# Optimization experiments

Hardware: AMD Instinct MI355X
Metric: run time of the kernel (lower is better)

## Reference

```python
import jax, jax.numpy as jnp
import numpy as np

B, N, DIM, H, DH = 2, 2048, 1024, 16, 64
INNER = H * DH
ROPE_BASE = 10000.0


def setup_inputs() -> dict:
    key = jax.random.key(0)
    ks = jax.random.split(key, 6)
    s = 0.02
    return {
        "x": jax.random.normal(ks[0], (B, N, DIM), jnp.float32),
        "Wq": jax.random.normal(ks[1], (DIM, INNER), jnp.float32) * s,
        "Wk": jax.random.normal(ks[2], (DIM, INNER), jnp.float32) * s,
        "Wv": jax.random.normal(ks[3], (DIM, INNER), jnp.float32) * s,
        "Wo": jax.random.normal(ks[4], (INNER, DIM), jnp.float32) * s,
        "bo": jnp.zeros((DIM,), jnp.float32),
    }


def _rotate_half(x):
    # einops '... (d r) -> ... d r' with r=2: x1 = even lanes, x2 = odd lanes,
    # then cat((-x2, x1), dim=-1)
    x1 = x[..., 0::2]
    x2 = x[..., 1::2]
    return jnp.concatenate([-x2, x1], axis=-1)


def _rope_sin_cos(n, d, dtype):
    # inv_freq over arange(0, d, 2); emb = cat(f, f) -> length d
    inv_freq = 1.0 / (ROPE_BASE ** (jnp.arange(0, d, 2, dtype=jnp.float32) / d))
    f = jnp.arange(n, dtype=jnp.float32)[:, None] * inv_freq[None, :]  # [n, d/2]
    e = jnp.concatenate([f, f], axis=-1)  # [n, d]
    return jnp.sin(e).astype(dtype), jnp.cos(e).astype(dtype)


def _apply_rope(t, sin, cos):
    # t: [b, h, n, d]; sin/cos: [n, d]; rot_dim == d (full head), t_pass empty
    return t * cos[None, None] + _rotate_half(t) * sin[None, None]


def reference(x, Wq, Wk, Wv, Wo, bo):
    b, n, _ = x.shape
    scale = DH ** (-0.5)

    def split_heads(y):  # [b, n, h*d] -> [b, h, n, d]
        return y.reshape(b, n, H, DH).transpose(0, 2, 1, 3)

    q = split_heads(x @ Wq)
    k = split_heads(x @ Wk)
    v = split_heads(x @ Wv)

    sin, cos = _rope_sin_cos(n, DH, x.dtype)
    q = _apply_rope(q, sin, cos)
    k = _apply_rope(k, sin, cos)

    # causal SDPA (mask=None path -> is_causal=True), eval mode so dropout_p=0
    scores = jnp.einsum("bhqd,bhkd->bhqk", q, k) * scale
    causal = jnp.tril(jnp.ones((n, n), dtype=bool))
    scores = jnp.where(causal[None, None], scores, jnp.finfo(scores.dtype).min)
    probs = jax.nn.softmax(scores, axis=-1)
    attn = jnp.einsum("bhqk,bhkd->bhqd", probs, v)

    out = attn.transpose(0, 2, 1, 3).reshape(b, n, INNER) @ Wo + bo
    return out, k, v
```

## Files before the change

### kernel.cpp

```cpp
#include <hip/hip_runtime.h>
#include <cstdint>
#include <cmath>

#define BB   2
#define NN   2048
#define DIMM 1024
#define NHH  16
#define DHH  64
#define MMR  (BB * NN)

typedef _Float16 half8  __attribute__((ext_vector_type(8)));
typedef _Float16 half4v __attribute__((ext_vector_type(4)));
typedef float    f32x4  __attribute__((ext_vector_type(4)));

#define GLD16(gp, lp)                                                          \
  __builtin_amdgcn_global_load_lds(                                            \
      (const __attribute__((address_space(1))) unsigned int*)(gp),             \
      (__attribute__((address_space(3))) unsigned int*)(lp), 16, 0, 0)

__global__ __launch_bounds__(256) void cvt_x_kernel(const float* __restrict__ x,
                                                    _Float16* __restrict__ xh) {
  int i = (blockIdx.x * 256 + threadIdx.x) * 4;
  float4 v = *(const float4*)(x + i);
  half4v h;
  h[0] = (_Float16)v.x; h[1] = (_Float16)v.y;
  h[2] = (_Float16)v.z; h[3] = (_Float16)v.w;
  *(half4v*)(xh + i) = h;
}

__global__ __launch_bounds__(256) void transpose_w_kernel(
    const float* __restrict__ Wq, const float* __restrict__ Wk,
    const float* __restrict__ Wv, const float* __restrict__ Wo,
    _Float16* __restrict__ wt) {
  __shared__ float tile[64][65];
  int z = blockIdx.z;
  const float* W = (z == 0) ? Wq : (z == 1) ? Wk : (z == 2) ? Wv : Wo;
  _Float16* dst = wt + (size_t)z * 1024 * 1024;
  int r0 = blockIdx.x * 64;
  int c0 = blockIdx.y * 64;
  int t = threadIdx.x;
  int tr = t >> 4;
  int tc = (t & 15) * 4;
#pragma unroll
  for (int i = 0; i < 4; ++i) {
    float4 v = *(const float4*)(W + (size_t)(r0 + tr + i * 16) * 1024 + c0 + tc);
    tile[tr + i * 16][tc + 0] = v.x;
    tile[tr + i * 16][tc + 1] = v.y;
    tile[tr + i * 16][tc + 2] = v.z;
    tile[tr + i * 16][tc + 3] = v.w;
  }
  __syncthreads();
#pragma unroll
  for (int i = 0; i < 4; ++i) {
    int nl = tr + i * 16;
    half4v hv;
    hv[0] = (_Float16)tile[tc + 0][nl];
    hv[1] = (_Float16)tile[tc + 1][nl];
    hv[2] = (_Float16)tile[tc + 2][nl];
    hv[3] = (_Float16)tile[tc + 3][nl];
    *(half4v*)(dst + (size_t)(c0 + nl) * 1024 + r0 + tc) = hv;
  }
}

__global__ __launch_bounds__(256) void gemm_qkv_kernel(
    const _Float16* __restrict__ xh, const _Float16* __restrict__ wt,
    float* __restrict__ ko, float* __restrict__ vo,
    _Float16* __restrict__ qh, _Float16* __restrict__ kh,
    _Float16* __restrict__ vth) {
  __shared__ __align__(16) _Float16 Ast[64 * 32];
  __shared__ __align__(16) _Float16 Bst[64 * 32];
  __shared__ float Cs[64][65];
  const int m0  = blockIdx.x * 64;
  const int ngl = blockIdx.y * 64;
  const int mat = ngl >> 10;
  const int n0  = ngl & 1023;
  const _Float16* wb = wt + (size_t)mat * 1024 * 1024;
  const int t = threadIdx.x;
  const int wv = t >> 6, lane = t & 63, l16 = lane & 15, quad = lane >> 4;
  const int r = t >> 2, cl = t & 3;
  const int c = cl ^ ((r >> 2) & 3);
  const _Float16* pa = xh + (size_t)(m0 + r) * 1024 + c * 8;
  const _Float16* pb = wb + (size_t)(n0 + r) * 1024 + c * 8;
  f32x4 acc[4] = {};
  const int arow = wv * 16 + l16;
  const int aoff = arow * 32 + (quad ^ ((arow >> 2) & 3)) * 8;
  for (int k0 = 0; k0 < 1024; k0 += 32) {
    __syncthreads();
    GLD16(pa + k0, Ast + wv * 512);
    GLD16(pb + k0, Bst + wv * 512);
    __syncthreads();
    half8 af = *(const half8*)(Ast + aoff);
#pragma unroll
    for (int nt = 0; nt < 4; ++nt) {
      int brow = nt * 16 + l16;
      half8 bf = *(const half8*)(Bst + brow * 32 + (quad ^ ((brow >> 2) & 3)) * 8);
      acc[nt] = __builtin_amdgcn_mfma_f32_16x16x32_f16(af, bf, acc[nt], 0, 0, 0);
    }
  }
#pragma unroll
  for (int nt = 0; nt < 4; ++nt)
#pragma unroll
    for (int rr = 0; rr < 4; ++rr)
      Cs[wv * 16 + quad * 4 + rr][nt * 16 + l16] = acc[nt][rr];
  __syncthreads();
  int lr = t >> 2;
  int cseg = (t & 3) * 16;
  int m = m0 + lr;
  int b = m >> 11;
  int pos = m & 2047;
  int h = n0 >> 6;
  int bhh = b * NHH + h;
  float vals[16];
  if (mat == 2) {
#pragma unroll
    for (int j = 0; j < 16; ++j) vals[j] = Cs[lr][cseg + j];
  } else {
    float fpos = (float)pos;
#pragma unroll
    for (int j = 0; j < 16; ++j) {
      int i = cseg + j;
      int jd = (i < 32) ? i : (i - 32);
      float invf = exp2f((float)jd * -0.41524101186092029f);
      float ang = fpos * invf;
      float sv, cv;
      sincosf(ang, &sv, &cv);
      float partner = (i < 32) ? -Cs[lr][2 * i + 1] : Cs[lr][2 * (i - 32)];
      vals[j] = Cs[lr][i] * cv + partner * sv;
    }
  }
  size_t rowb = ((size_t)bhh * NN + pos) * DHH + cseg;
  if (mat == 0) {
    half8 h0, h1;
#pragma unroll
    for (int j = 0; j < 8; ++j) { h0[j] = (_Float16)(vals[j] * 0.125f); h1[j] = (_Float16)(vals[8 + j] * 0.125f); }
    *(half8*)(qh + rowb) = h0;
    *(half8*)(qh + rowb + 8) = h1;
  } else if (mat == 1) {
#pragma unroll
    for (int j4 = 0; j4 < 4; ++j4) {
      float4 o;
      o.x = vals[j4 * 4 + 0]; o.y = vals[j4 * 4 + 1];
      o.z = vals[j4 * 4 + 2]; o.w = vals[j4 * 4 + 3];
      *(float4*)(ko + rowb + j4 * 4) = o;
    }
    half8 h0, h1;
#pragma unroll
    for (int j = 0; j < 8; ++j) { h0[j] = (_Float16)vals[j]; h1[j] = (_Float16)vals[8 + j]; }
    *(half8*)(kh + rowb) = h0;
    *(half8*)(kh + rowb + 8) = h1;
  } else {
#pragma unroll
    for (int j4 = 0; j4 < 4; ++j4) {
      float4 o;
      o.x = vals[j4 * 4 + 0]; o.y = vals[j4 * 4 + 1];
      o.z = vals[j4 * 4 + 2]; o.w = vals[j4 * 4 + 3];
      *(float4*)(vo + rowb + j4 * 4) = o;
    }
#pragma unroll
    for (int j = 0; j < 16; ++j)
      vth[((size_t)bhh * DHH + cseg + j) * NN + pos] = (_Float16)vals[j];
  }
}

__global__ __launch_bounds__(256, 2) void fattn_kernel(
    const _Float16* __restrict__ qh, const _Float16* __restrict__ kh,
    const _Float16* __restrict__ vth, _Float16* __restrict__ ah) {
  __shared__ __align__(16) _Float16 Kt[2][4096];
  __shared__ __align__(16) _Float16 Vt[2][4096];
  __shared__ __align__(16) _Float16 Pb[4][16][72];
  const int qb = 15 - (int)blockIdx.x;
  const int bh = blockIdx.y;
  const int t = threadIdx.x;
  const int wv = t >> 6, lane = t & 63, l16 = lane & 15, quad = lane >> 4;
  const int q0 = qb * 128;
  const _Float16* kg = kh + (size_t)bh * NN * DHH;
  const _Float16* vg = vth + (size_t)bh * DHH * NN;
  half8 qf[2][2];
#pragma unroll
  for (int qt2 = 0; qt2 < 2; ++qt2) {
    const _Float16* qp =
        qh + ((size_t)bh * NN + q0 + wv * 32 + qt2 * 16 + l16) * DHH + quad * 8;
    qf[qt2][0] = *(const half8*)qp;
    qf[qt2][1] = *(const half8*)(qp + 32);
  }
  half8 ones;
#pragma unroll
  for (int j = 0; j < 8; ++j) ones[j] = (_Float16)1.f;
  f32x4 o[2][4] = {};
  f32x4 ls[2] = {};
  const int ktmax = 2 * qb + 1;
#pragma unroll
  for (int iss = 0; iss < 2; ++iss) {
    int cid = iss * 256 + wv * 64 + lane;
    int row = cid >> 3;
    int c = (cid & 7) ^ (row & 7);
    GLD16(kg + (size_t)row * DHH + c * 8, &Kt[0][(iss * 256 + wv * 64) * 8]);
    GLD16(vg + (size_t)row * NN + c * 8, &Vt[0][(iss * 256 + wv * 64) * 8]);
  }
  int cur = 0;
  for (int kt = 0; kt <= ktmax; ++kt) {
    __syncthreads();
    if (kt < ktmax) {
      const _Float16* kn = kg + (size_t)(kt + 1) * 64 * DHH;
      const _Float16* vn = vg + (kt + 1) * 64;
      int nb = cur ^ 1;
#pragma unroll
      for (int iss = 0; iss < 2; ++iss) {
        int cid = iss * 256 + wv * 64 + lane;
        int row = cid >> 3;
        int c = (cid & 7) ^ (row & 7);
        GLD16(kn + (size_t)row * DHH + c * 8, &Kt[nb][(iss * 256 + wv * 64) * 8]);
        GLD16(vn + (size_t)row * NN + c * 8, &Vt[nb][(iss * 256 + wv * 64) * 8]);
      }
    }
    if (kt * 64 <= q0 + wv * 32 + 31) {
      half8 kf[4][2], vf[4][2];
      const _Float16* Kb = Kt[cur];
      const _Float16* Vb = Vt[cur];
#pragma unroll
      for (int nt = 0; nt < 4; ++nt) {
        int row = nt * 16 + l16;
        int r7 = row & 7;
        kf[nt][0] = *(const half8*)(Kb + row * 64 + ((quad ^ r7) * 8));
        kf[nt][1] = *(const half8*)(Kb + row * 64 + (((quad + 4) ^ r7) * 8));
        vf[nt][0] = *(const half8*)(Vb + row * 64 + ((quad ^ r7) * 8));
        vf[nt][1] = *(const half8*)(Vb + row * 64 + (((quad + 4) ^ r7) * 8));
      }
#pragma unroll
      for (int qt2 = 0; qt2 < 2; ++qt2) {
        int base = q0 + wv * 32 + qt2 * 16;
        if (kt * 64 <= base + 15) {
          f32x4 s4[4];
#pragma unroll
          for (int nt = 0; nt < 4; ++nt) {
            f32x4 z = {};
            z = __builtin_amdgcn_mfma_f32_16x16x32_f16(qf[qt2][0], kf[nt][0], z, 0, 0, 0);
            s4[nt] = __builtin_amdgcn_mfma_f32_16x16x32_f16(qf[qt2][1], kf[nt][1], z, 0, 0, 0);
          }
          if (kt * 64 + 63 > base) {
#pragma unroll
            for (int nt = 0; nt < 4; ++nt) {
              int key = kt * 64 + nt * 16 + l16;
#pragma unroll
              for (int r = 0; r < 4; ++r) {
                float p = (key > base + quad * 4 + r) ? 0.f : __expf(s4[nt][r]);
                Pb[wv][quad * 4 + r][nt * 16 + l16] = (_Float16)p;
              }
            }
          } else {
#pragma unroll
            for (int nt = 0; nt < 4; ++nt)
#pragma unroll
              for (int r = 0; r < 4; ++r)
                Pb[wv][quad * 4 + r][nt * 16 + l16] = (_Float16)__expf(s4[nt][r]);
          }
          asm volatile("s_waitcnt lgkmcnt(0)" ::: "memory");
          half8 pf0 = *(const half8*)&Pb[wv][l16][quad * 8];
          half8 pf1 = *(const half8*)&Pb[wv][l16][32 + quad * 8];
#pragma unroll
          for (int nt = 0; nt < 4; ++nt) {
            o[qt2][nt] = __builtin_amdgcn_mfma_f32_16x16x32_f16(pf0, vf[nt][0], o[qt2][nt], 0, 0, 0);
            o[qt2][nt] = __builtin_amdgcn_mfma_f32_16x16x32_f16(pf1, vf[nt][1], o[qt2][nt], 0, 0, 0);
          }
          ls[qt2] = __builtin_amdgcn_mfma_f32_16x16x32_f16(pf0, ones, ls[qt2], 0, 0, 0);
          ls[qt2] = __builtin_amdgcn_mfma_f32_16x16x32_f16(pf1, ones, ls[qt2], 0, 0, 0);
        }
      }
    }
    cur ^= 1;
  }
  const int b = bh >> 4, h = bh & 15;
#pragma unroll
  for (int qt2 = 0; qt2 < 2; ++qt2)
#pragma unroll
    for (int r = 0; r < 4; ++r) {
      float inv = 1.f / ls[qt2][r];
      int pos = q0 + wv * 32 + qt2 * 16 + quad * 4 + r;
      size_t ob = ((size_t)(b * NN + pos)) * DIMM + h * DHH;
#pragma unroll
      for (int nt = 0; nt < 4; ++nt)
        ah[ob + nt * 16 + l16] = (_Float16)(o[qt2][nt][r] * inv);
    }
}

__global__ __launch_bounds__(256) void gemm_out_kernel(
    const _Float16* __restrict__ ah, const _Float16* __restrict__ wot,
    const float* __restrict__ bo, float* __restrict__ out) {
  __shared__ __align__(16) _Float16 Ast[64 * 32];
  __shared__ __align__(16) _Float16 Bst[64 * 32];
  const int m0 = blockIdx.x * 64;
  const int n0 = blockIdx.y * 64;
  const int t = threadIdx.x;
  const int wv = t >> 6, lane = t & 63, l16 = lane & 15, quad = lane >> 4;
  const int r = t >> 2, cl = t & 3;
  const int c = cl ^ ((r >> 2) & 3);
  const _Float16* pa = ah + (size_t)(m0 + r) * 1024 + c * 8;
  const _Float16* pb = wot + (size_t)(n0 + r) * 1024 + c * 8;
  f32x4 acc[4] = {};
  const int arow = wv * 16 + l16;
  const int aoff = arow * 32 + (quad ^ ((arow >> 2) & 3)) * 8;
  for (int k0 = 0; k0 < 1024; k0 += 32) {
    __syncthreads();
    GLD16(pa + k0, Ast + wv * 512);
    GLD16(pb + k0, Bst + wv * 512);
    __syncthreads();
    half8 af = *(const half8*)(Ast + aoff);
#pragma unroll
    for (int nt = 0; nt < 4; ++nt) {
      int brow = nt * 16 + l16;
      half8 bf = *(const half8*)(Bst + brow * 32 + (quad ^ ((brow >> 2) & 3)) * 8);
      acc[nt] = __builtin_amdgcn_mfma_f32_16x16x32_f16(af, bf, acc[nt], 0, 0, 0);
    }
  }
#pragma unroll
  for (int nt = 0; nt < 4; ++nt) {
    int col = n0 + nt * 16 + l16;
    float bias = bo[col];
#pragma unroll
    for (int rr = 0; rr < 4; ++rr) {
      out[(size_t)(m0 + wv * 16 + quad * 4 + rr) * 1024 + col] = acc[nt][rr] + bias;
    }
  }
}

extern "C" void kernel_launch(void* const* d_in, const int* in_sizes, int n_in,
                              void* d_out, int out_size, void* d_ws, size_t ws_size,
                              hipStream_t stream) {
  (void)in_sizes; (void)n_in; (void)out_size; (void)ws_size;
  const float* x  = (const float*)d_in[0];
  const float* Wq = (const float*)d_in[1];
  const float* Wk = (const float*)d_in[2];
  const float* Wv = (const float*)d_in[3];
  const float* Wo = (const float*)d_in[4];
  const float* bo = (const float*)d_in[5];

  float* out = (float*)d_out;
  float* ko  = out + (size_t)MMR * DIMM;
  float* vo  = ko + (size_t)BB * NHH * NN * DHH;

  char* w = (char*)d_ws;
  _Float16* xh  = (_Float16*)w;
  _Float16* ah  = (_Float16*)w;
  _Float16* wt  = (_Float16*)(w + (8u << 20));
  _Float16* qh  = (_Float16*)(w + (16u << 20));
  _Float16* kh  = (_Float16*)(w + (24u << 20));
  _Float16* vth = (_Float16*)(w + (32u << 20));

  hipLaunchKernelGGL(cvt_x_kernel, dim3(4096), dim3(256), 0, stream, x, xh);
  hipLaunchKernelGGL(transpose_w_kernel, dim3(16, 16, 4), dim3(256), 0, stream,
                     Wq, Wk, Wv, Wo, wt);
  hipLaunchKernelGGL(gemm_qkv_kernel, dim3(64, 48), dim3(256), 0, stream,
                     xh, wt, ko, vo, qh, kh, vth);
  hipLaunchKernelGGL(fattn_kernel, dim3(16, 32), dim3(256), 0, stream,
                     qh, kh, vth, ah);
  hipLaunchKernelGGL(gemm_out_kernel, dim3(64, 16), dim3(256), 0, stream,
                     ah, wt + (size_t)3 * 1024 * 1024, bo, out);
}
```

Measured before the change: 235.1 us.

## Enlarge QKV and output GEMM tiles to 128x128 with 2x2 wave layout

Both GEMM kernels move from 64x64 block tiles, where each wave computes 16x64, to 128x128 block tiles, where each wave computes a 64x64 sub-tile with a 4x4 grid of MFMA accumulators. This raises arithmetic intensity per LDS load and per global fetch. The QKV epilogue now shares LDS with the staging buffers and runs two head-chunk passes so RoPE and the layout scatter still fit. The cost is more registers per thread, fewer blocks (768 and 256), lower occupancy and weaker wave-level parallelism on a large-CU GPU. The K loop is still single-buffered.

```diff
diff --git a/kernel.cpp b/kernel.cpp
--- a/kernel.cpp
+++ b/kernel.cpp
@@ -67,98 +67,124 @@
     float* __restrict__ ko, float* __restrict__ vo,
     _Float16* __restrict__ qh, _Float16* __restrict__ kh,
     _Float16* __restrict__ vth) {
-  __shared__ __align__(16) _Float16 Ast[64 * 32];
-  __shared__ __align__(16) _Float16 Bst[64 * 32];
-  __shared__ float Cs[64][65];
-  const int m0  = blockIdx.x * 64;
-  const int ngl = blockIdx.y * 64;
-  const int mat = ngl >> 10;
-  const int n0  = ngl & 1023;
+  __shared__ __align__(16) char smem[128 * 65 * 4];
+  _Float16* Ast = (_Float16*)smem;
+  _Float16* Bst = (_Float16*)(smem + 8192);
+  float (*Cs)[65] = (float(*)[65])smem;
+
+  const int m0  = blockIdx.x * 128;
+  const int mat = blockIdx.y >> 3;
+  const int n0  = (blockIdx.y & 7) * 128;
   const _Float16* wb = wt + (size_t)mat * 1024 * 1024;
   const int t = threadIdx.x;
   const int wv = t >> 6, lane = t & 63, l16 = lane & 15, quad = lane >> 4;
+  const int wr = wv >> 1, wc = wv & 1;
   const int r = t >> 2, cl = t & 3;
   const int c = cl ^ ((r >> 2) & 3);
   const _Float16* pa = xh + (size_t)(m0 + r) * 1024 + c * 8;
   const _Float16* pb = wb + (size_t)(n0 + r) * 1024 + c * 8;
-  f32x4 acc[4] = {};
-  const int arow = wv * 16 + l16;
-  const int aoff = arow * 32 + (quad ^ ((arow >> 2) & 3)) * 8;
+  f32x4 acc[4][4] = {};
+  int aoffs[4], boffs[4];
+#pragma unroll
+  for (int mi = 0; mi < 4; ++mi) {
+    int arow = wr * 64 + mi * 16 + l16;
+    aoffs[mi] = arow * 32 + (quad ^ ((arow >> 2) & 3)) * 8;
+  }
+#pragma unroll
+  for (int n = 0; n < 4; ++n) {
+    int brow = wc * 64 + n * 16 + l16;
+    boffs[n] = brow * 32 + (quad ^ ((brow >> 2) & 3)) * 8;
+  }
   for (int k0 = 0; k0 < 1024; k0 += 32) {
     __syncthreads();
     GLD16(pa + k0, Ast + wv * 512);
+    GLD16(pa + 64 * 1024 + k0, Ast + 2048 + wv * 512);
     GLD16(pb + k0, Bst + wv * 512);
-    __syncthreads();
-    half8 af = *(const half8*)(Ast + aoff);
-#pragma unroll
-    for (int nt = 0; nt < 4; ++nt) {
-      int brow = nt * 16 + l16;
-      half8 bf = *(const half8*)(Bst + brow * 32 + (quad ^ ((brow >> 2) & 3)) * 8);
-      acc[nt] = __builtin_amdgcn_mfma_f32_16x16x32_f16(af, bf, acc[nt], 0, 0, 0);
-    }
-  }
-#pragma unroll
-  for (int nt = 0; nt < 4; ++nt)
-#pragma unroll
-    for (int rr = 0; rr < 4; ++rr)
-      Cs[wv * 16 + quad * 4 + rr][nt * 16 + l16] = acc[nt][rr];
-  __syncthreads();
-  int lr = t >> 2;
-  int cseg = (t & 3) * 16;
-  int m = m0 + lr;
-  int b = m >> 11;
-  int pos = m & 2047;
-  int h = n0 >> 6;
-  int bhh = b * NHH + h;
-  float vals[16];
-  if (mat == 2) {
-#pragma unroll
-    for (int j = 0; j < 16; ++j) vals[j] = Cs[lr][cseg + j];
-  } else {
-    float fpos = (float)pos;
-#pragma unroll
-    for (int j = 0; j < 16; ++j) {
-      int i = cseg + j;
-      int jd = (i < 32) ? i : (i - 32);
-      float invf = exp2f((float)jd * -0.41524101186092029f);
-      float ang = fpos * invf;
-      float sv, cv;
-      sincosf(ang, &sv, &cv);
-      float partner = (i < 32) ? -Cs[lr][2 * i + 1] : Cs[lr][2 * (i - 32)];
-      vals[j] = Cs[lr][i] * cv + partner * sv;
-    }
-  }
-  size_t rowb = ((size_t)bhh * NN + pos) * DHH + cseg;
-  if (mat == 0) {
-    half8 h0, h1;
-#pragma unroll
-    for (int j = 0; j < 8; ++j) { h0[j] = (_Float16)(vals[j] * 0.125f); h1[j] = (_Float16)(vals[8 + j] * 0.125f); }
-    *(half8*)(qh + rowb) = h0;
-    *(half8*)(qh + rowb + 8) = h1;
-  } else if (mat == 1) {
-#pragma unroll
-    for (int j4 = 0; j4 < 4; ++j4) {
-      float4 o;
-      o.x = vals[j4 * 4 + 0]; o.y = vals[j4 * 4 + 1];
-      o.z = vals[j4 * 4 + 2]; o.w = vals[j4 * 4 + 3];
-      *(float4*)(ko + rowb + j4 * 4) = o;
-    }
-    half8 h0, h1;
-#pragma unroll
-    for (int j = 0; j < 8; ++j) { h0[j] = (_Float16)vals[j]; h1[j] = (_Float16)vals[8 + j]; }
-    *(half8*)(kh + rowb) = h0;
-    *(half8*)(kh + rowb + 8) = h1;
-  } else {
-#pragma unroll
-    for (int j4 = 0; j4 < 4; ++j4) {
-      float4 o;
-      o.x = vals[j4 * 4 + 0]; o.y = vals[j4 * 4 + 1];
-      o.z = vals[j4 * 4 + 2]; o.w = vals[j4 * 4 + 3];
-      *(float4*)(vo + rowb + j4 * 4) = o;
-    }
-#pragma unroll
-    for (int j = 0; j < 16; ++j)
-      vth[((size_t)bhh * DHH + cseg + j) * NN + pos] = (_Float16)vals[j];
+    GLD16(pb + 64 * 1024 + k0, Bst + 2048 + wv * 512);
+    __syncthreads();
+    half8 af[4], bf[4];
+#pragma unroll
+    for (int mi = 0; mi < 4; ++mi) af[mi] = *(const half8*)(Ast + aoffs[mi]);
+#pragma unroll
+    for (int n = 0; n < 4; ++n) bf[n] = *(const half8*)(Bst + boffs[n]);
+#pragma unroll
+    for (int mi = 0; mi < 4; ++mi)
+#pragma unroll
+      for (int n = 0; n < 4; ++n)
+        acc[mi][n] = __builtin_amdgcn_mfma_f32_16x16x32_f16(af[mi], bf[n], acc[mi][n], 0, 0, 0);
+  }
+  const int lr = t >> 1;
+  const int cseg = (t & 1) * 32;
+  const int m = m0 + lr;
+  const int b = m >> 11;
+  const int pos = m & 2047;
+  const float fpos = (float)pos;
+  for (int ch = 0; ch < 2; ++ch) {
+    __syncthreads();
+    if (wc == ch) {
+#pragma unroll
+      for (int mi = 0; mi < 4; ++mi)
+#pragma unroll
+        for (int n = 0; n < 4; ++n)
+#pragma unroll
+          for (int rr = 0; rr < 4; ++rr)
+            Cs[wr * 64 + mi * 16 + quad * 4 + rr][n * 16 + l16] = acc[mi][n][rr];
+    }
+    __syncthreads();
+    const int h = (n0 >> 6) + ch;
+    const int bhh = b * NHH + h;
+    float vals[32];
+    if (mat == 2) {
+#pragma unroll
+      for (int j = 0; j < 32; ++j) vals[j] = Cs[lr][cseg + j];
+    } else {
+      const bool lo = (cseg == 0);
+#pragma unroll
+      for (int j = 0; j < 32; ++j) {
+        float invf = exp2f((float)j * -0.41524101186092029f);
+        float ang = fpos * invf;
+        float sv, cv;
+        sincosf(ang, &sv, &cv);
+        float partner = lo ? -Cs[lr][2 * j + 1] : Cs[lr][2 * j];
+        vals[j] = Cs[lr][cseg + j] * cv + partner * sv;
+      }
+    }
+    size_t rowb = ((size_t)bhh * NN + pos) * DHH + cseg;
+    if (mat == 0) {
+#pragma unroll
+      for (int j8 = 0; j8 < 4; ++j8) {
+        half8 hv;
+#pragma unroll
+        for (int j = 0; j < 8; ++j) hv[j] = (_Float16)(vals[j8 * 8 + j] * 0.125f);
+        *(half8*)(qh + rowb + j8 * 8) = hv;
+      }
+    } else if (mat == 1) {
+#pragma unroll
+      for (int j4 = 0; j4 < 8; ++j4) {
+        float4 o;
+        o.x = vals[j4 * 4 + 0]; o.y = vals[j4 * 4 + 1];
+        o.z = vals[j4 * 4 + 2]; o.w = vals[j4 * 4 + 3];
+        *(float4*)(ko + rowb + j4 * 4) = o;
+      }
+#pragma unroll
+      for (int j8 = 0; j8 < 4; ++j8) {
+        half8 hv;
+#pragma unroll
+        for (int j = 0; j < 8; ++j) hv[j] = (_Float16)vals[j8 * 8 + j];
+        *(half8*)(kh + rowb + j8 * 8) = hv;
+      }
+    } else {
+#pragma unroll
+      for (int j4 = 0; j4 < 8; ++j4) {
+        float4 o;
+        o.x = vals[j4 * 4 + 0]; o.y = vals[j4 * 4 + 1];
+        o.z = vals[j4 * 4 + 2]; o.w = vals[j4 * 4 + 3];
+        *(float4*)(vo + rowb + j4 * 4) = o;
+      }
+#pragma unroll
+      for (int j = 0; j < 32; ++j)
+        vth[((size_t)bhh * DHH + cseg + j) * NN + pos] = (_Float16)vals[j];
+    }
   }
 }
 
@@ -286,41 +312,58 @@
 __global__ __launch_bounds__(256) void gemm_out_kernel(
     const _Float16* __restrict__ ah, const _Float16* __restrict__ wot,
     const float* __restrict__ bo, float* __restrict__ out) {
-  __shared__ __align__(16) _Float16 Ast[64 * 32];
-  __shared__ __align__(16) _Float16 Bst[64 * 32];
-  const int m0 = blockIdx.x * 64;
-  const int n0 = blockIdx.y * 64;
+  __shared__ __align__(16) _Float16 Ast[128 * 32];
+  __shared__ __align__(16) _Float16 Bst[128 * 32];
+  const int m0 = blockIdx.x * 128;
+  const int n0 = blockIdx.y * 128;
   const int t = threadIdx.x;
   const int wv = t >> 6, lane = t & 63, l16 = lane & 15, quad = lane >> 4;
+  const int wr = wv >> 1, wc = wv & 1;
   const int r = t >> 2, cl = t & 3;
   const int c = cl ^ ((r >> 2) & 3);
   const _Float16* pa = ah + (size_t)(m0 + r) * 1024 + c * 8;
   const _Float16* pb = wot + (size_t)(n0 + r) * 1024 + c * 8;
-  f32x4 acc[4] = {};
-  const int arow = wv * 16 + l16;
-  const int aoff = arow * 32 + (quad ^ ((arow >> 2) & 3)) * 8;
+  f32x4 acc[4][4] = {};
+  int aoffs[4], boffs[4];
+#pragma unroll
+  for (int mi = 0; mi < 4; ++mi) {
+    int arow = wr * 64 + mi * 16 + l16;
+    aoffs[mi] = arow * 32 + (quad ^ ((arow >> 2) & 3)) * 8;
+  }
+#pragma unroll
+  for (int n = 0; n < 4; ++n) {
+    int brow = wc * 64 + n * 16 + l16;
+    boffs[n] = brow * 32 + (quad ^ ((brow >> 2) & 3)) * 8;
+  }
   for (int k0 = 0; k0 < 1024; k0 += 32) {
     __syncthreads();
     GLD16(pa + k0, Ast + wv * 512);
+    GLD16(pa + 64 * 1024 + k0, Ast + 2048 + wv * 512);
     GLD16(pb + k0, Bst + wv * 512);
-    __syncthreads();
-    half8 af = *(const half8*)(Ast + aoff);
-#pragma unroll
-    for (int nt = 0; nt < 4; ++nt) {
-      int brow = nt * 16 + l16;
-      half8 bf = *(const half8*)(Bst + brow * 32 + (quad ^ ((brow >> 2) & 3)) * 8);
-      acc[nt] = __builtin_amdgcn_mfma_f32_16x16x32_f16(af, bf, acc[nt], 0, 0, 0);
-    }
-  }
-#pragma unroll
-  for (int nt = 0; nt < 4; ++nt) {
-    int col = n0 + nt * 16 + l16;
-    float bias = bo[col];
-#pragma unroll
-    for (int rr = 0; rr < 4; ++rr) {
-      out[(size_t)(m0 + wv * 16 + quad * 4 + rr) * 1024 + col] = acc[nt][rr] + bias;
-    }
-  }
+    GLD16(pb + 64 * 1024 + k0, Bst + 2048 + wv * 512);
+    __syncthreads();
+    half8 af[4], bf[4];
+#pragma unroll
+    for (int mi = 0; mi < 4; ++mi) af[mi] = *(const half8*)(Ast + aoffs[mi]);
+#pragma unroll
+    for (int n = 0; n < 4; ++n) bf[n] = *(const half8*)(Bst + boffs[n]);
+#pragma unroll
+    for (int mi = 0; mi < 4; ++mi)
+#pragma unroll
+      for (int n = 0; n < 4; ++n)
+        acc[mi][n] = __builtin_amdgcn_mfma_f32_16x16x32_f16(af[mi], bf[n], acc[mi][n], 0, 0, 0);
+  }
+#pragma unroll
+  for (int mi = 0; mi < 4; ++mi)
+#pragma unroll
+    for (int n = 0; n < 4; ++n) {
+      int col = n0 + wc * 64 + n * 16 + l16;
+      float bias = bo[col];
+#pragma unroll
+      for (int rr = 0; rr < 4; ++rr)
+        out[(size_t)(m0 + wr * 64 + mi * 16 + quad * 4 + rr) * 1024 + col] =
+            acc[mi][n][rr] + bias;
+    }
 }
 
 extern "C" void kernel_launch(void* const* d_in, const int* in_sizes, int n_in,
@@ -349,10 +392,10 @@
   hipLaunchKernelGGL(cvt_x_kernel, dim3(4096), dim3(256), 0, stream, x, xh);
   hipLaunchKernelGGL(transpose_w_kernel, dim3(16, 16, 4), dim3(256), 0, stream,
                      Wq, Wk, Wv, Wo, wt);
-  hipLaunchKernelGGL(gemm_qkv_kernel, dim3(64, 48), dim3(256), 0, stream,
+  hipLaunchKernelGGL(gemm_qkv_kernel, dim3(32, 24), dim3(256), 0, stream,
                      xh, wt, ko, vo, qh, kh, vth);
   hipLaunchKernelGGL(fattn_kernel, dim3(16, 32), dim3(256), 0, stream,
                      qh, kh, vth, ah);
-  hipLaunchKernelGGL(gemm_out_kernel, dim3(64, 16), dim3(256), 0, stream,
+  hipLaunchKernelGGL(gemm_out_kernel, dim3(32, 8), dim3(256), 0, stream,
                      ah, wt + (size_t)3 * 1024 * 1024, bo, out);
 }
```

Measured after the change: 274.4 us. 1.17x slower.

## Double-buffer GEMM K-tiles with async LDS loads and wider K step

Applied to the files above, without the earlier changes.

Both the QKV projection and output GEMM kernels now use a two-stage LDS ping-pong buffer. The next 64-wide K slice is fetched via global_load_lds while MFMAs consume the current one, with explicit vmcnt waits and raw barriers replacing the two __syncthreads per 32-wide step. The K step doubles, which halves loop iterations and barriers, and the LDS swizzle changes to an 8-way XOR. This costs 32KB of LDS per block, which may reduce occupancy, and relies on hand-placed waitcnt correctness.

```diff
diff --git a/kernel.cpp b/kernel.cpp
--- a/kernel.cpp
+++ b/kernel.cpp
@@ -67,9 +67,11 @@
     float* __restrict__ ko, float* __restrict__ vo,
     _Float16* __restrict__ qh, _Float16* __restrict__ kh,
     _Float16* __restrict__ vth) {
-  __shared__ __align__(16) _Float16 Ast[64 * 32];
-  __shared__ __align__(16) _Float16 Bst[64 * 32];
-  __shared__ float Cs[64][65];
+  __shared__ __align__(16) char smem[32768];
+  _Float16* As = (_Float16*)smem;
+  _Float16* Bs = (_Float16*)(smem + 16384);
+  float (*Cs)[65] = (float(*)[65])smem;
+
   const int m0  = blockIdx.x * 64;
   const int ngl = blockIdx.y * 64;
   const int mat = ngl >> 10;
@@ -77,25 +79,51 @@
   const _Float16* wb = wt + (size_t)mat * 1024 * 1024;
   const int t = threadIdx.x;
   const int wv = t >> 6, lane = t & 63, l16 = lane & 15, quad = lane >> 4;
-  const int r = t >> 2, cl = t & 3;
-  const int c = cl ^ ((r >> 2) & 3);
-  const _Float16* pa = xh + (size_t)(m0 + r) * 1024 + c * 8;
-  const _Float16* pb = wb + (size_t)(n0 + r) * 1024 + c * 8;
+  const int r  = t >> 3;
+  const int cl = t & 7;
+  const int csw = (cl ^ (r & 7)) * 8;
+  const _Float16* pa0 = xh + (size_t)(m0 + r) * 1024 + csw;
+  const _Float16* pa1 = pa0 + 32 * 1024;
+  const _Float16* pb0 = wb + (size_t)(n0 + r) * 1024 + csw;
+  const _Float16* pb1 = pb0 + 32 * 1024;
   f32x4 acc[4] = {};
   const int arow = wv * 16 + l16;
-  const int aoff = arow * 32 + (quad ^ ((arow >> 2) & 3)) * 8;
-  for (int k0 = 0; k0 < 1024; k0 += 32) {
-    __syncthreads();
-    GLD16(pa + k0, Ast + wv * 512);
-    GLD16(pb + k0, Bst + wv * 512);
-    __syncthreads();
-    half8 af = *(const half8*)(Ast + aoff);
+  const int a7 = arow & 7;
+  GLD16(pa0, As + wv * 512);
+  GLD16(pa1, As + 2048 + wv * 512);
+  GLD16(pb0, Bs + wv * 512);
+  GLD16(pb1, Bs + 2048 + wv * 512);
+  int cur = 0;
+  for (int k0 = 0; k0 < 1024; k0 += 64) {
+    if (k0 + 64 < 1024) {
+      const int nb = cur ^ 1;
+      GLD16(pa0 + k0 + 64, As + nb * 4096 + wv * 512);
+      GLD16(pa1 + k0 + 64, As + nb * 4096 + 2048 + wv * 512);
+      GLD16(pb0 + k0 + 64, Bs + nb * 4096 + wv * 512);
+      GLD16(pb1 + k0 + 64, Bs + nb * 4096 + 2048 + wv * 512);
+      asm volatile("s_waitcnt vmcnt(4)" ::: "memory");
+    } else {
+      asm volatile("s_waitcnt vmcnt(0)" ::: "memory");
+    }
+    __builtin_amdgcn_s_barrier();
+    asm volatile("" ::: "memory");
+    const _Float16* Ab = As + cur * 4096;
+    const _Float16* Bb = Bs + cur * 4096;
+    half8 af0 = *(const half8*)(Ab + arow * 64 + (quad ^ a7) * 8);
+    half8 af1 = *(const half8*)(Ab + arow * 64 + ((4 + quad) ^ a7) * 8);
 #pragma unroll
     for (int nt = 0; nt < 4; ++nt) {
       int brow = nt * 16 + l16;
-      half8 bf = *(const half8*)(Bst + brow * 32 + (quad ^ ((brow >> 2) & 3)) * 8);
-      acc[nt] = __builtin_amdgcn_mfma_f32_16x16x32_f16(af, bf, acc[nt], 0, 0, 0);
-    }
+      int b7 = brow & 7;
+      half8 bf0 = *(const half8*)(Bb + brow * 64 + (quad ^ b7) * 8);
+      half8 bf1 = *(const half8*)(Bb + brow * 64 + ((4 + quad) ^ b7) * 8);
+      acc[nt] = __builtin_amdgcn_mfma_f32_16x16x32_f16(af0, bf0, acc[nt], 0, 0, 0);
+      acc[nt] = __builtin_amdgcn_mfma_f32_16x16x32_f16(af1, bf1, acc[nt], 0, 0, 0);
+    }
+    asm volatile("s_waitcnt lgkmcnt(0)" ::: "memory");
+    __builtin_amdgcn_s_barrier();
+    asm volatile("" ::: "memory");
+    cur ^= 1;
   }
 #pragma unroll
   for (int nt = 0; nt < 4; ++nt)
@@ -286,31 +314,58 @@
 __global__ __launch_bounds__(256) void gemm_out_kernel(
     const _Float16* __restrict__ ah, const _Float16* __restrict__ wot,
     const float* __restrict__ bo, float* __restrict__ out) {
-  __shared__ __align__(16) _Float16 Ast[64 * 32];
-  __shared__ __align__(16) _Float16 Bst[64 * 32];
+  __shared__ __align__(16) char smem[32768];
+  _Float16* As = (_Float16*)smem;
+  _Float16* Bs = (_Float16*)(smem + 16384);
   const int m0 = blockIdx.x * 64;
   const int n0 = blockIdx.y * 64;
   const int t = threadIdx.x;
   const int wv = t >> 6, lane = t & 63, l16 = lane & 15, quad = lane >> 4;
-  const int r = t >> 2, cl = t & 3;
-  const int c = cl ^ ((r >> 2) & 3);
-  const _Float16* pa = ah + (size_t)(m0 + r) * 1024 + c * 8;
-  const _Float16* pb = wot + (size_t)(n0 + r) * 1024 + c * 8;
+  const int r  = t >> 3;
+  const int cl = t & 7;
+  const int csw = (cl ^ (r & 7)) * 8;
+  const _Float16* pa0 = ah + (size_t)(m0 + r) * 1024 + csw;
+  const _Float16* pa1 = pa0 + 32 * 1024;
+  const _Float16* pb0 = wot + (size_t)(n0 + r) * 1024 + csw;
+  const _Float16* pb1 = pb0 + 32 * 1024;
   f32x4 acc[4] = {};
   const int arow = wv * 16 + l16;
-  const int aoff = arow * 32 + (quad ^ ((arow >> 2) & 3)) * 8;
-  for (int k0 = 0; k0 < 1024; k0 += 32) {
-    __syncthreads();
-    GLD16(pa + k0, Ast + wv * 512);
-    GLD16(pb + k0, Bst + wv * 512);
-    __syncthreads();
-    half8 af = *(const half8*)(Ast + aoff);
+  const int a7 = arow & 7;
+  GLD16(pa0, As + wv * 512);
+  GLD16(pa1, As + 2048 + wv * 512);
+  GLD16(pb0, Bs + wv * 512);
+  GLD16(pb1, Bs + 2048 + wv * 512);
+  int cur = 0;
+  for (int k0 = 0; k0 < 1024; k0 += 64) {
+    if (k0 + 64 < 1024) {
+      const int nb = cur ^ 1;
+      GLD16(pa0 + k0 + 64, As + nb * 4096 + wv * 512);
+      GLD16(pa1 + k0 + 64, As + nb * 4096 + 2048 + wv * 512);
+      GLD16(pb0 + k0 + 64, Bs + nb * 4096 + wv * 512);
+      GLD16(pb1 + k0 + 64, Bs + nb * 4096 + 2048 + wv * 512);
+      asm volatile("s_waitcnt vmcnt(4)" ::: "memory");
+    } else {
+      asm volatile("s_waitcnt vmcnt(0)" ::: "memory");
+    }
+    __builtin_amdgcn_s_barrier();
+    asm volatile("" ::: "memory");
+    const _Float16* Ab = As + cur * 4096;
+    const _Float16* Bb = Bs + cur * 4096;
+    half8 af0 = *(const half8*)(Ab + arow * 64 + (quad ^ a7) * 8);
+    half8 af1 = *(const half8*)(Ab + arow * 64 + ((4 + quad) ^ a7) * 8);
 #pragma unroll
     for (int nt = 0; nt < 4; ++nt) {
       int brow = nt * 16 + l16;
-      half8 bf = *(const half8*)(Bst + brow * 32 + (quad ^ ((brow >> 2) & 3)) * 8);
-      acc[nt] = __builtin_amdgcn_mfma_f32_16x16x32_f16(af, bf, acc[nt], 0, 0, 0);
-    }
+      int b7 = brow & 7;
+      half8 bf0 = *(const half8*)(Bb + brow * 64 + (quad ^ b7) * 8);
+      half8 bf1 = *(const half8*)(Bb + brow * 64 + ((4 + quad) ^ b7) * 8);
+      acc[nt] = __builtin_amdgcn_mfma_f32_16x16x32_f16(af0, bf0, acc[nt], 0, 0, 0);
+      acc[nt] = __builtin_amdgcn_mfma_f32_16x16x32_f16(af1, bf1, acc[nt], 0, 0, 0);
+    }
+    asm volatile("s_waitcnt lgkmcnt(0)" ::: "memory");
+    __builtin_amdgcn_s_barrier();
+    asm volatile("" ::: "memory");
+    cur ^= 1;
   }
 #pragma unroll
   for (int nt = 0; nt < 4; ++nt) {
```

Result: faster. 211.1 us (-10.2%).
